# Kernel tuning notes

Hardware: AMD Instinct MI355X
Metric: run time of the kernel (lower is better)

Reference implementation:

```python
import jax, jax.numpy as jnp
import numpy as np


def setup_inputs() -> dict:
    key = jax.random.key(0)
    kx, ky = jax.random.split(key)
    B, C, D, H, W = 2, 16, 64, 128, 128
    x = jax.random.normal(kx, (B, C, D, H, W), dtype=jnp.float32)
    y = jax.random.randint(ky, (B, D, H, W), 0, C, dtype=jnp.int64)
    return {"x": x, "y": y}


def reference(x, y):
    # x: [B,C,D,H,W] logits, y: [B,D,H,W] int labels in [0,C)
    B, C = x.shape[0], x.shape[1]
    logp = jax.nn.log_softmax(x, axis=1)                      # [B,C,D,H,W]
    # per-voxel NLL = CrossEntropyLoss(reduction='none')
    nll = -jnp.take_along_axis(logp, y[:, None], axis=1)[:, 0]  # [B,D,H,W]

    # fuse the B*C masked means into one segment reduction over (b, class)
    nll_flat = nll.reshape(-1)                                # [B*N]
    seg = (jnp.arange(B, dtype=y.dtype)[:, None] * C + y.reshape(B, -1)).reshape(-1)
    sums = jax.ops.segment_sum(nll_flat, seg, num_segments=B * C)
    counts = jax.ops.segment_sum(jnp.ones_like(nll_flat), seg, num_segments=B * C)
    # classes absent in a sample contribute 0 (matches `if m.any()`)
    means = jnp.where(counts > 0, sums / jnp.maximum(counts, 1.0), 0.0)  # [B*C]
    r = means.reshape(B, C).sum(axis=1) / C                   # [B]
    return r.mean()
```

## Files before the change

kernel.cpp:

```cpp
#include <hip/hip_runtime.h>

#define BB 2
#define CC 16
#define NVOX (64 * 128 * 128)
#define N4   (NVOX / 4)

__global__ void cwce_init(float* __restrict__ ws_sum, unsigned* __restrict__ ws_cnt) {
    int t = threadIdx.x;
    if (t < BB * CC) { ws_sum[t] = 0.0f; ws_cnt[t] = 0u; }
}

__global__ __launch_bounds__(256) void cwce_main(const float* __restrict__ x,
                                                 const int* __restrict__ y,
                                                 float* __restrict__ ws_sum,
                                                 unsigned* __restrict__ ws_cnt) {
    __shared__ float    s_sum[CC];
    __shared__ unsigned s_cnt[CC];
    const int t = threadIdx.x;
    if (t < CC) { s_sum[t] = 0.0f; s_cnt[t] = 0u; }
    __syncthreads();

    const unsigned gid = blockIdx.x * 256u + t;
    const unsigned b   = gid >> 18;
    const unsigned n4  = gid & (N4 - 1);

    const float4* xb = (const float4*)x + (size_t)(b * CC) * N4 + n4;
    const int4 lab4 = ((const int4*)y)[gid];

    float xv[CC][4];
#pragma unroll
    for (int c = 0; c < CC; ++c) {
        float4 v = xb[(size_t)c * N4];
        xv[c][0] = v.x; xv[c][1] = v.y; xv[c][2] = v.z; xv[c][3] = v.w;
    }
    const int labs[4] = {lab4.x, lab4.y, lab4.z, lab4.w};

#pragma unroll
    for (int j = 0; j < 4; ++j) {
        float m = xv[0][j];
#pragma unroll
        for (int c = 1; c < CC; ++c) m = fmaxf(m, xv[c][j]);
        const int lj = labs[j];
        float s = 0.0f, xy = 0.0f;
#pragma unroll
        for (int c = 0; c < CC; ++c) {
            s += __expf(xv[c][j] - m);
            if (c == lj) xy = xv[c][j];
        }
        const float nll = m + __logf(s) - xy;
        atomicAdd(&s_sum[lj], nll);
        atomicAdd(&s_cnt[lj], 1u);
    }
    __syncthreads();

    if (t < CC) {
        atomicAdd(&ws_sum[b * CC + t], s_sum[t]);
        atomicAdd(&ws_cnt[b * CC + t], s_cnt[t]);
    }
}

__global__ void cwce_final(const float* __restrict__ ws_sum,
                           const unsigned* __restrict__ ws_cnt,
                           float* __restrict__ out) {
    const int t = threadIdx.x;
    float v = 0.0f;
    if (t < BB * CC) {
        const unsigned c = ws_cnt[t];
        v = (c > 0u) ? (ws_sum[t] / (float)c) : 0.0f;
    }
#pragma unroll
    for (int off = 32; off >= 1; off >>= 1) v += __shfl_down(v, off);
    if (t == 0) out[0] = v * (1.0f / (BB * CC));
}

extern "C" void kernel_launch(void* const* d_in, const int* in_sizes, int n_in,
                              void* d_out, int out_size, void* d_ws, size_t ws_size,
                              hipStream_t stream) {
    const float* x = (const float*)d_in[0];
    const int*   y = (const int*)d_in[1];
    float*       out = (float*)d_out;

    float*    ws_sum = (float*)d_ws;
    unsigned* ws_cnt = (unsigned*)(ws_sum + BB * CC);

    cwce_init<<<1, 64, 0, stream>>>(ws_sum, ws_cnt);
    cwce_main<<<2048, 256, 0, stream>>>(x, y, ws_sum, ws_cnt);
    cwce_final<<<1, 64, 0, stream>>>(ws_sum, ws_cnt, out);
}
```

Measured before the change: 199.9 us.

## Replace atomic class histograms with per-thread accumulators and two-stage deterministic reduction

Drops the shared-memory atomics per voxel and the global atomics per block. Each thread now keeps 16-class sum and count accumulators in registers, reduces them with wave shuffles, combines the waves in shared memory, and writes per-block partials to workspace. The final kernel reduces these partials, so the init kernel is no longer needed. The cost is more registers and 128 shuffles per thread, with a launch-bounds occupancy hint, and counts are now accumulated as floats.

```diff
diff --git a/kernel.cpp b/kernel.cpp
--- a/kernel.cpp
+++ b/kernel.cpp
@@ -4,21 +4,13 @@
 #define CC 16
 #define NVOX (64 * 128 * 128)
 #define N4   (NVOX / 4)
+#define NBLK 2048
 
-__global__ void cwce_init(float* __restrict__ ws_sum, unsigned* __restrict__ ws_cnt) {
-    int t = threadIdx.x;
-    if (t < BB * CC) { ws_sum[t] = 0.0f; ws_cnt[t] = 0u; }
-}
-
-__global__ __launch_bounds__(256) void cwce_main(const float* __restrict__ x,
-                                                 const int* __restrict__ y,
-                                                 float* __restrict__ ws_sum,
-                                                 unsigned* __restrict__ ws_cnt) {
-    __shared__ float    s_sum[CC];
-    __shared__ unsigned s_cnt[CC];
+__global__ __launch_bounds__(256, 4) void cwce_main(const float* __restrict__ x,
+                                                    const int* __restrict__ y,
+                                                    float* __restrict__ ws) {
+    __shared__ float s_part[4][2 * CC];
     const int t = threadIdx.x;
-    if (t < CC) { s_sum[t] = 0.0f; s_cnt[t] = 0u; }
-    __syncthreads();
 
     const unsigned gid = blockIdx.x * 256u + t;
     const unsigned b   = gid >> 18;
@@ -35,6 +27,11 @@
     }
     const int labs[4] = {lab4.x, lab4.y, lab4.z, lab4.w};
 
+    float acc_s[CC];
+    float acc_c[CC];
+#pragma unroll
+    for (int c = 0; c < CC; ++c) { acc_s[c] = 0.0f; acc_c[c] = 0.0f; }
+
 #pragma unroll
     for (int j = 0; j < 4; ++j) {
         float m = xv[0][j];
@@ -48,29 +45,75 @@
             if (c == lj) xy = xv[c][j];
         }
         const float nll = m + __logf(s) - xy;
-        atomicAdd(&s_sum[lj], nll);
-        atomicAdd(&s_cnt[lj], 1u);
+#pragma unroll
+        for (int c = 0; c < CC; ++c) {
+            const bool hit = (c == lj);
+            acc_s[c] += hit ? nll : 0.0f;
+            acc_c[c] += hit ? 1.0f : 0.0f;
+        }
+    }
+
+#pragma unroll
+    for (int c = 0; c < CC; ++c) {
+#pragma unroll
+        for (int off = 32; off >= 1; off >>= 1) {
+            acc_s[c] += __shfl_down(acc_s[c], off);
+            acc_c[c] += __shfl_down(acc_c[c], off);
+        }
+    }
+
+    const int wave = t >> 6;
+    if ((t & 63) == 0) {
+#pragma unroll
+        for (int c = 0; c < CC; ++c) {
+            s_part[wave][c]      = acc_s[c];
+            s_part[wave][CC + c] = acc_c[c];
+        }
     }
     __syncthreads();
 
-    if (t < CC) {
-        atomicAdd(&ws_sum[b * CC + t], s_sum[t]);
-        atomicAdd(&ws_cnt[b * CC + t], s_cnt[t]);
+    if (t < 2 * CC) {
+        float p = s_part[0][t] + s_part[1][t] + s_part[2][t] + s_part[3][t];
+        ws[blockIdx.x * (2 * CC) + t] = p;
     }
 }
 
-__global__ void cwce_final(const float* __restrict__ ws_sum,
-                           const unsigned* __restrict__ ws_cnt,
-                           float* __restrict__ out) {
+__global__ __launch_bounds__(256) void cwce_final(const float* __restrict__ ws,
+                                                  float* __restrict__ out) {
+    __shared__ float sb[BB][8][2 * CC];
     const int t = threadIdx.x;
-    float v = 0.0f;
-    if (t < BB * CC) {
-        const unsigned c = ws_cnt[t];
-        v = (c > 0u) ? (ws_sum[t] / (float)c) : 0.0f;
+    const int k = t & 31;
+    const int g = t >> 5;
+
+    float a0 = 0.0f, a1 = 0.0f;
+    for (int blk = g; blk < NBLK / 2; blk += 8)            a0 += ws[blk * 32 + k];
+    for (int blk = NBLK / 2 + g; blk < NBLK; blk += 8)     a1 += ws[blk * 32 + k];
+    sb[0][g][k] = a0;
+    sb[1][g][k] = a1;
+    __syncthreads();
+
+    if (t < 64) {
+        const int b  = t >> 5;
+        const int kk = t & 31;
+        float tot = 0.0f;
+#pragma unroll
+        for (int gg = 0; gg < 8; ++gg) tot += sb[b][gg][kk];
+        sb[b][0][kk] = tot;
     }
+    __syncthreads();
+
+    if (t < 64) {
+        float v = 0.0f;
+        if (t < BB * CC) {
+            const int b = t >> 4, c = t & 15;
+            const float sum = sb[b][0][c];
+            const float cnt = sb[b][0][CC + c];
+            v = (cnt > 0.0f) ? (sum / cnt) : 0.0f;
+        }
 #pragma unroll
-    for (int off = 32; off >= 1; off >>= 1) v += __shfl_down(v, off);
-    if (t == 0) out[0] = v * (1.0f / (BB * CC));
+        for (int off = 32; off >= 1; off >>= 1) v += __shfl_down(v, off);
+        if (t == 0) out[0] = v * (1.0f / (BB * CC));
+    }
 }
 
 extern "C" void kernel_launch(void* const* d_in, const int* in_sizes, int n_in,
@@ -79,11 +122,8 @@
     const float* x = (const float*)d_in[0];
     const int*   y = (const int*)d_in[1];
     float*       out = (float*)d_out;
+    float*       ws  = (float*)d_ws;
 
-    float*    ws_sum = (float*)d_ws;
-    unsigned* ws_cnt = (unsigned*)(ws_sum + BB * CC);
-
-    cwce_init<<<1, 64, 0, stream>>>(ws_sum, ws_cnt);
-    cwce_main<<<2048, 256, 0, stream>>>(x, y, ws_sum, ws_cnt);
-    cwce_final<<<1, 64, 0, stream>>>(ws_sum, ws_cnt, out);
+    cwce_main<<<NBLK, 256, 0, stream>>>(x, y, ws);
+    cwce_final<<<1, 256, 0, stream>>>(ws, out);
 }
```

Measured after the change: 261.4 us. +30.8%, slower.
